# Kernel tuning notes

Measured on AMD Instinct MI355X. Metric: run time of the kernel, lower is better.

The kernel has to match this reference:

```python
import jax, jax.numpy as jnp
import numpy as np

B, N, C, H = 4, 2048, 768, 12
D = C // H  # head_dim = 64

def setup_inputs() -> dict:
    key = jax.random.key(0)
    ks = jax.random.split(key, 6)
    s = 0.02
    return {
        "img_tokens": jax.random.normal(ks[0], (B, N, C), jnp.float32),
        "ln_gamma": jnp.ones((C,), jnp.float32),
        "ln_beta": jnp.zeros((C,), jnp.float32),
        "w_qkv": jax.random.normal(ks[1], (C, 3 * C), jnp.float32) * s,
        "w_out": jax.random.normal(ks[2], (C, C), jnp.float32) * s,
        "b_out": jnp.zeros((C,), jnp.float32),
    }

def reference(img_tokens, ln_gamma, ln_beta, w_qkv, w_out, b_out):
    x = img_tokens
    # LayerNorm over channel dim
    mu = jnp.mean(x, axis=-1, keepdims=True)
    var = jnp.var(x, axis=-1, keepdims=True)
    xn = (x - mu) * jax.lax.rsqrt(var + 1e-5) * ln_gamma + ln_beta
    qkv = xn @ w_qkv                      # [B, N, 3C]
    q, k, v = jnp.split(qkv, 3, axis=-1)
    def heads(t):                          # [B, N, C] -> [B, H, N, D]
        return t.reshape(B, N, H, D).transpose(0, 2, 1, 3)
    q, k, v = heads(q), heads(k), heads(v)
    scale = 1.0 / np.sqrt(D).astype(np.float32)
    scores = jnp.einsum('bhnd,bhmd->bhnm', q, k) * scale  # [B, H, N, N]
    attn = jax.nn.softmax(scores, axis=-1)
    out = jnp.einsum('bhnm,bhmd->bhnd', attn, v)          # [B, H, N, D]
    out = out.transpose(0, 2, 1, 3).reshape(B, N, C)
    out = out @ w_out + b_out
    return out + img_tokens
```

## Files before the change

kernel.cpp:

```cpp
#include <hip/hip_runtime.h>


typedef __bf16 bf16x8 __attribute__((ext_vector_type(8)));
typedef float  f32x4  __attribute__((ext_vector_type(4)));

#define MFMA16(a,b,c) __builtin_amdgcn_mfma_f32_16x16x32_bf16((a),(b),(c),0,0,0)

__device__ inline f32x4 zero4() { f32x4 z = {0.f,0.f,0.f,0.f}; return z; }

__device__ inline void gll16(const __bf16* g, __bf16* l) {
  __builtin_amdgcn_global_load_lds((const __attribute__((address_space(1))) unsigned int*)g,
                                   (__attribute__((address_space(3))) unsigned int*)l,
                                   16, 0, 0);
}

__device__ inline __bf16 bf16_trunc(float f) {
  const unsigned int u = __builtin_bit_cast(unsigned int, f);
  return __builtin_bit_cast(__bf16, (unsigned short)(u >> 16));
}

__global__ __launch_bounds__(256) void ln_kernel(const float* __restrict__ x,
                                                 const float* __restrict__ g,
                                                 const float* __restrict__ bt,
                                                 __bf16* __restrict__ xn) {
  const int row = blockIdx.x;
  const int tid = threadIdx.x;
  const float* xr = x + (size_t)row * 768;
  float v[3]; float s = 0.f, ss = 0.f;
  #pragma unroll
  for (int i = 0; i < 3; ++i) { float f = xr[tid + 256*i]; v[i] = f; s += f; ss += f*f; }
  #pragma unroll
  for (int m = 32; m >= 1; m >>= 1) { s += __shfl_xor(s, m, 64); ss += __shfl_xor(ss, m, 64); }
  __shared__ float red[8];
  const int wave = tid >> 6;
  if ((tid & 63) == 0) { red[wave] = s; red[4 + wave] = ss; }
  __syncthreads();
  s  = red[0] + red[1] + red[2] + red[3];
  ss = red[4] + red[5] + red[6] + red[7];
  const float mu  = s * (1.f/768.f);
  const float var = ss * (1.f/768.f) - mu*mu;
  const float inv = rsqrtf(var + 1e-5f);
  __bf16* xo = xn + (size_t)row * 768;
  #pragma unroll
  for (int i = 0; i < 3; ++i) {
    const int c0 = tid + 256*i;
    xo[c0] = (__bf16)((v[i] - mu) * inv * g[c0] + bt[c0]);
  }
}

__global__ __launch_bounds__(256) void transpose_kernel(const float* __restrict__ in,
                                                        __bf16* __restrict__ out,
                                                        int R, int C) {
  __shared__ float t[32][33];
  const int tx = threadIdx.x & 31, ty = threadIdx.x >> 5;
  const int c0 = blockIdx.x * 32, r0 = blockIdx.y * 32;
  #pragma unroll
  for (int p = 0; p < 4; ++p) t[ty + 8*p][tx] = in[(size_t)(r0 + ty + 8*p) * C + c0 + tx];
  __syncthreads();
  #pragma unroll
  for (int p = 0; p < 4; ++p) out[(size_t)(c0 + ty + 8*p) * R + r0 + tx] = (__bf16)t[tx][ty + 8*p];
}

template<int KDIM>
__device__ inline void gemm_mainloop(const __bf16* __restrict__ A, const __bf16* __restrict__ BT,
                                     int bm, int bn, int wave, int lane,
                                     f32x4 acc[4][4], __bf16* Asm, __bf16* Bsm) {
  const int wm = wave >> 1, wn = wave & 1;
  const int lr = lane & 15, lk = lane >> 4;
  for (int k0 = 0; k0 < KDIM; k0 += 64) {
    #pragma unroll
    for (int s2 = 0; s2 < 4; ++s2) {
      const int st = wave * 4 + s2;
      const int rb = st >> 1, kh = st & 1;
      gll16(A  + (size_t)(bm + rb*16 + lr) * KDIM + k0 + kh*32 + lk*8, Asm + st*512);
      gll16(BT + (size_t)(bn + rb*16 + lr) * KDIM + k0 + kh*32 + lk*8, Bsm + st*512);
    }
    __builtin_amdgcn_s_waitcnt(0);
    __syncthreads();
    #pragma unroll
    for (int ks = 0; ks < 2; ++ks) {
      bf16x8 a[4], b[4];
      #pragma unroll
      for (int mt = 0; mt < 4; ++mt) a[mt] = *(const bf16x8*)(Asm + ((wm*4+mt)*2+ks)*512 + lane*8);
      #pragma unroll
      for (int nt = 0; nt < 4; ++nt) b[nt] = *(const bf16x8*)(Bsm + ((wn*4+nt)*2+ks)*512 + lane*8);
      #pragma unroll
      for (int mt = 0; mt < 4; ++mt)
        #pragma unroll
        for (int nt = 0; nt < 4; ++nt)
          acc[mt][nt] = MFMA16(a[mt], b[nt], acc[mt][nt]);
    }
    __syncthreads();
  }
}

__global__ __launch_bounds__(256) void gemm_qkv_kernel(const __bf16* __restrict__ A,
                                                       const __bf16* __restrict__ BT,
                                                       __bf16* __restrict__ q,
                                                       __bf16* __restrict__ k,
                                                       __bf16* __restrict__ vt) {
  __shared__ __align__(16) __bf16 smem[2*8192];
  __bf16* Asm = smem;
  __bf16* Bsm = smem + 8192;
  const int lane = threadIdx.x & 63, wave = threadIdx.x >> 6;
  const int bm = blockIdx.y * 128, bn = blockIdx.x * 128;
  f32x4 acc[4][4];
  #pragma unroll
  for (int i = 0; i < 4; ++i)
    #pragma unroll
    for (int j = 0; j < 4; ++j) acc[i][j] = zero4();
  gemm_mainloop<768>(A, BT, bm, bn, wave, lane, acc, Asm, Bsm);
  const int wm = wave >> 1, wn = wave & 1;
  const int quad = lane >> 4, c = lane & 15;
  if (bn < 1536) {
    const float qscale = 0.125f * 1.44269504088896f;
    #pragma unroll
    for (int mt = 0; mt < 4; ++mt)
      #pragma unroll
      for (int nt = 0; nt < 4; ++nt) {
        const int col = bn + wn*64 + nt*16 + c;
        const int which = col >= 768 ? 1 : 0;
        const int within = col - which*768;
        const int h = within >> 6, d = within & 63;
        #pragma unroll
        for (int r = 0; r < 4; ++r) {
          const int row = bm + wm*64 + mt*16 + quad*4 + r;
          const int b = row >> 11, n = row & 2047;
          const float vv = acc[mt][nt][r];
          const size_t idx = ((size_t)(b*12 + h) * 2048 + n) * 64 + d;
          if (which == 0) q[idx] = (__bf16)(vv * qscale);
          else            k[idx] = (__bf16)vv;
        }
      }
  } else {
    __syncthreads();
    #pragma unroll
    for (int mt = 0; mt < 4; ++mt)
      #pragma unroll
      for (int nt = 0; nt < 4; ++nt) {
        const int lcol = wn*64 + nt*16 + c;
        #pragma unroll
        for (int r = 0; r < 4; ++r) {
          const int lrow = wm*64 + mt*16 + quad*4 + r;
          smem[lrow*66 + lcol] = (__bf16)acc[mt][nt][r];
        }
      }
    __syncthreads();
    const int b = bm >> 11, n0 = bm & 2047;
    const int vo = bn - 1536;
    const int n = threadIdx.x & 127;
    const int csel = threadIdx.x >> 7;
    #pragma unroll
    for (int pass = 0; pass < 64; ++pass) {
      const int lc = pass*2 + csel;
      const int gcol = vo + lc;
      const int h = gcol >> 6, d = gcol & 63;
      vt[((size_t)(b*12 + h)*64 + d)*2048 + n0 + n] = smem[n*66 + lc];
    }
  }
}

__global__ __launch_bounds__(256) void gemm_out_kernel(const __bf16* __restrict__ A,
                                                       const __bf16* __restrict__ BT,
                                                       const float* __restrict__ bias,
                                                       const float* __restrict__ resid,
                                                       float* __restrict__ out) {
  __shared__ __align__(16) __bf16 Asm[16*512];
  __shared__ __align__(16) __bf16 Bsm[16*512];
  const int lane = threadIdx.x & 63, wave = threadIdx.x >> 6;
  const int bm = blockIdx.y * 128, bn = blockIdx.x * 128;
  f32x4 acc[4][4];
  #pragma unroll
  for (int i = 0; i < 4; ++i)
    #pragma unroll
    for (int j = 0; j < 4; ++j) acc[i][j] = zero4();
  gemm_mainloop<768>(A, BT, bm, bn, wave, lane, acc, Asm, Bsm);
  const int wm = wave >> 1, wn = wave & 1;
  const int quad = lane >> 4, c = lane & 15;
  #pragma unroll
  for (int mt = 0; mt < 4; ++mt)
    #pragma unroll
    for (int nt = 0; nt < 4; ++nt) {
      const int col = bn + wn*64 + nt*16 + c;
      #pragma unroll
      for (int r = 0; r < 4; ++r) {
        const int row = bm + wm*64 + mt*16 + quad*4 + r;
        out[(size_t)row*768 + col] = acc[mt][nt][r] + bias[col] + resid[(size_t)row*768 + col];
      }
    }
}

__global__ __launch_bounds__(256) void attn_kernel(const __bf16* __restrict__ q,
                                                   const __bf16* __restrict__ k,
                                                   const __bf16* __restrict__ vt,
                                                   __bf16* __restrict__ o) {
  const int xcd = blockIdx.x & 7, i = blockIdx.x >> 3;
  const int bh = xcd * 6 + (i >> 4);
  const int qt = i & 15;
  const int lane = threadIdx.x & 63, wave = threadIdx.x >> 6;
  const int c = lane & 15, quad = lane >> 4;
  const int lr = lane & 15, lk = lane >> 4;
  const int q0 = qt*128 + wave*32;

  const __bf16* qb = q  + ((size_t)bh*2048 + q0) * 64;
  const __bf16* kb = k  + (size_t)bh * 2048 * 64;
  const __bf16* vb = vt + (size_t)bh * 64 * 2048;

  __shared__ __align__(16) __bf16 Ksm[2][4096];
  __shared__ __align__(16) __bf16 Vsm[2][4096];
  __shared__ __align__(16) __bf16 plds[4][1024];
  __bf16* myp = plds[wave];

  bf16x8 aq[2][2];
  #pragma unroll
  for (int rg = 0; rg < 2; ++rg) {
    aq[rg][0] = *(const bf16x8*)(qb + (size_t)(rg*16 + c)*64 + quad*8);
    aq[rg][1] = *(const bf16x8*)(qb + (size_t)(rg*16 + c)*64 + 32 + quad*8);
  }

  float cl[2][4];
  f32x4 od[2][4];
  #pragma unroll
  for (int rg = 0; rg < 2; ++rg)
    #pragma unroll
    for (int r = 0; r < 4; ++r) { cl[rg][r] = 0.f; od[rg][r] = zero4(); }

  auto stage = [&](int it) {
    const int kt = it * 64;
    __bf16* Ks = Ksm[it & 1];
    __bf16* Vs = Vsm[it & 1];
    gll16(kb + (size_t)(kt + wave*16 + lr) * 64 + lk*8,        Ks + (wave*2+0)*512);
    gll16(kb + (size_t)(kt + wave*16 + lr) * 64 + 32 + lk*8,   Ks + (wave*2+1)*512);
    gll16(vb + (size_t)(wave*16 + lr) * 2048 + kt + lk*8,      Vs + (wave*2+0)*512);
    gll16(vb + (size_t)(wave*16 + lr) * 2048 + kt + 32 + lk*8, Vs + (wave*2+1)*512);
  };

  stage(0);
  stage(1);

  const int sl = lane ^ ((lane >> 3) & 7);

  for (int it = 0; it < 32; ++it) {
    const __bf16* Ks = Ksm[it & 1];
    const __bf16* Vs = Vsm[it & 1];
    if (it < 31) asm volatile("s_waitcnt vmcnt(4)" ::: "memory");
    else         asm volatile("s_waitcnt vmcnt(0)" ::: "memory");
    asm volatile("s_barrier" ::: "memory");
    #pragma unroll
    for (int ch = 0; ch < 2; ++ch) {
      f32x4 s0[2], s1[2];
      #pragma unroll
      for (int t2 = 0; t2 < 2; ++t2) {
        const int t = ch*2 + t2;
        const bf16x8 b0 = *(const bf16x8*)(Ks + (t*2+0)*512 + lane*8);
        const bf16x8 b1 = *(const bf16x8*)(Ks + (t*2+1)*512 + lane*8);
        f32x4 z0 = zero4(), z1 = zero4();
        z0 = MFMA16(aq[0][0], b0, z0); z0 = MFMA16(aq[0][1], b1, z0);
        z1 = MFMA16(aq[1][0], b0, z1); z1 = MFMA16(aq[1][1], b1, z1);
        s0[t2] = z0; s1[t2] = z1;
      }
      #pragma unroll
      for (int t2 = 0; t2 < 2; ++t2) {
        const int kk = t2*16 + c;
        const int k8 = kk >> 3, j = kk & 7;
        #pragma unroll
        for (int r = 0; r < 4; ++r) {
          const int row = quad*4 + r;
          const int b = k8*16 + row;
          const int sb = b ^ ((b >> 3) & 7);
          const float p0 = __builtin_amdgcn_exp2f(s0[t2][r]);
          const float p1 = __builtin_amdgcn_exp2f(s1[t2][r]);
          cl[0][r] += p0; cl[1][r] += p1;
          myp[sb*8 + j]       = bf16_trunc(p0);
          myp[512 + sb*8 + j] = bf16_trunc(p1);
        }
      }
      asm volatile("s_waitcnt lgkmcnt(0)" ::: "memory");
      const bf16x8 ap0 = *(const bf16x8*)(myp + sl*8);
      const bf16x8 ap1 = *(const bf16x8*)(myp + 512 + sl*8);
      asm volatile("" ::: "memory");
      #pragma unroll
      for (int dt = 0; dt < 4; ++dt) {
        const bf16x8 bv = *(const bf16x8*)(Vs + (dt*2+ch)*512 + lane*8);
        od[0][dt] = MFMA16(ap0, bv, od[0][dt]);
        od[1][dt] = MFMA16(ap1, bv, od[1][dt]);
      }
    }
    asm volatile("s_barrier" ::: "memory");
    if (it + 2 < 32) stage(it + 2);
  }
  const int b = bh / 12, h = bh % 12;
  #pragma unroll
  for (int rg = 0; rg < 2; ++rg) {
    float rl[4];
    #pragma unroll
    for (int r = 0; r < 4; ++r) {
      float v0 = cl[rg][r];
      v0 += __shfl_xor(v0, 1); v0 += __shfl_xor(v0, 2);
      v0 += __shfl_xor(v0, 4); v0 += __shfl_xor(v0, 8);
      rl[r] = 1.f / v0;
    }
    #pragma unroll
    for (int dt = 0; dt < 4; ++dt)
      #pragma unroll
      for (int r = 0; r < 4; ++r) {
        const int n = q0 + rg*16 + quad*4 + r;
        const int col = h*64 + dt*16 + c;
        o[((size_t)b*2048 + n)*768 + col] = (__bf16)(od[rg][dt][r] * rl[r]);
      }
  }
}

extern "C" void kernel_launch(void* const* d_in, const int* in_sizes, int n_in,
                              void* d_out, int out_size, void* d_ws, size_t ws_size,
                              hipStream_t stream) {
  const float* img   = (const float*)d_in[0];
  const float* gamma = (const float*)d_in[1];
  const float* beta  = (const float*)d_in[2];
  const float* wqkv  = (const float*)d_in[3];
  const float* wout  = (const float*)d_in[4];
  const float* bout  = (const float*)d_in[5];
  float* out = (float*)d_out;

  __bf16* ws = (__bf16*)d_ws;
  size_t off = 0;
  __bf16* xn    = ws + off; off += (size_t)8192*768;
  __bf16* wqkvT = ws + off; off += (size_t)2304*768;
  __bf16* woutT = ws + off; off += (size_t)768*768;
  __bf16* qs    = ws + off; off += (size_t)48*2048*64;
  __bf16* ks    = ws + off; off += (size_t)48*2048*64;
  __bf16* vts   = ws + off; off += (size_t)48*64*2048;
  __bf16* os    = ws + off; off += (size_t)8192*768;

  ln_kernel<<<8192, 256, 0, stream>>>(img, gamma, beta, xn);
  transpose_kernel<<<dim3(72, 24), 256, 0, stream>>>(wqkv, wqkvT, 768, 2304);
  transpose_kernel<<<dim3(24, 24), 256, 0, stream>>>(wout, woutT, 768, 768);
  gemm_qkv_kernel<<<dim3(18, 64), 256, 0, stream>>>(xn, wqkvT, qs, ks, vts);
  attn_kernel<<<768, 256, 0, stream>>>(qs, ks, vts, os);
  gemm_out_kernel<<<dim3(6, 64), 256, 0, stream>>>(os, woutT, bout, img, out);
}
```

Before: 272.0 us.

## Keep softmax probabilities in registers via transposed QK MFMA and permlane swaps

Swaps the MFMA operand order for Q·K^T so each lane holds scores for one query row across consecutive keys. The probabilities are then packed to bf16 with v_cvt_pk_bf16_f32 and moved into the A-operand layout of the PV MFMA with permlane32/16 swaps. This drops the per-wave LDS round trip (scattered stores, lgkmcnt wait, reload) and the scratch LDS buffer. The row-sum reduction is also reorganized to a single accumulator per row group with cross-quad shuffles. Rounding changes from truncation to round-to-nearest, and the permlane mapping must match the MFMA operand layout exactly.

```diff
diff --git a/kernel.cpp b/kernel.cpp
--- a/kernel.cpp
+++ b/kernel.cpp
@@ -3,6 +3,7 @@
 
 typedef __bf16 bf16x8 __attribute__((ext_vector_type(8)));
 typedef float  f32x4  __attribute__((ext_vector_type(4)));
+typedef unsigned int u32x4 __attribute__((ext_vector_type(4)));
 
 #define MFMA16(a,b,c) __builtin_amdgcn_mfma_f32_16x16x32_bf16((a),(b),(c),0,0,0)
 
@@ -14,9 +15,16 @@
                                    16, 0, 0);
 }
 
-__device__ inline __bf16 bf16_trunc(float f) {
-  const unsigned int u = __builtin_bit_cast(unsigned int, f);
-  return __builtin_bit_cast(__bf16, (unsigned short)(u >> 16));
+__device__ inline unsigned cvt_pk_bf16(float lo, float hi) {
+  unsigned r;
+  asm("v_cvt_pk_bf16_f32 %0, %1, %2" : "=v"(r) : "v"(lo), "v"(hi));
+  return r;
+}
+__device__ inline void permlane32_swap(unsigned &a, unsigned &b) {
+  asm("v_permlane32_swap_b32 %0, %1" : "+v"(a), "+v"(b));
+}
+__device__ inline void permlane16_swap(unsigned &a, unsigned &b) {
+  asm("v_permlane16_swap_b32 %0, %1" : "+v"(a), "+v"(b));
 }
 
 __global__ __launch_bounds__(256) void ln_kernel(const float* __restrict__ x,
@@ -208,8 +216,6 @@
 
   __shared__ __align__(16) __bf16 Ksm[2][4096];
   __shared__ __align__(16) __bf16 Vsm[2][4096];
-  __shared__ __align__(16) __bf16 plds[4][1024];
-  __bf16* myp = plds[wave];
 
   bf16x8 aq[2][2];
   #pragma unroll
@@ -218,12 +224,14 @@
     aq[rg][1] = *(const bf16x8*)(qb + (size_t)(rg*16 + c)*64 + 32 + quad*8);
   }
 
-  float cl[2][4];
+  float cl[2];
   f32x4 od[2][4];
   #pragma unroll
-  for (int rg = 0; rg < 2; ++rg)
-    #pragma unroll
-    for (int r = 0; r < 4; ++r) { cl[rg][r] = 0.f; od[rg][r] = zero4(); }
+  for (int rg = 0; rg < 2; ++rg) {
+    cl[rg] = 0.f;
+    #pragma unroll
+    for (int r = 0; r < 4; ++r) od[rg][r] = zero4();
+  }
 
   auto stage = [&](int it) {
     const int kt = it * 64;
@@ -238,8 +246,6 @@
   stage(0);
   stage(1);
 
-  const int sl = lane ^ ((lane >> 3) & 7);
-
   for (int it = 0; it < 32; ++it) {
     const __bf16* Ks = Ksm[it & 1];
     const __bf16* Vs = Vsm[it & 1];
@@ -248,42 +254,43 @@
     asm volatile("s_barrier" ::: "memory");
     #pragma unroll
     for (int ch = 0; ch < 2; ++ch) {
-      f32x4 s0[2], s1[2];
+      unsigned pk[2][2][2];
       #pragma unroll
       for (int t2 = 0; t2 < 2; ++t2) {
         const int t = ch*2 + t2;
-        const bf16x8 b0 = *(const bf16x8*)(Ks + (t*2+0)*512 + lane*8);
-        const bf16x8 b1 = *(const bf16x8*)(Ks + (t*2+1)*512 + lane*8);
-        f32x4 z0 = zero4(), z1 = zero4();
-        z0 = MFMA16(aq[0][0], b0, z0); z0 = MFMA16(aq[0][1], b1, z0);
-        z1 = MFMA16(aq[1][0], b0, z1); z1 = MFMA16(aq[1][1], b1, z1);
-        s0[t2] = z0; s1[t2] = z1;
-      }
-      #pragma unroll
-      for (int t2 = 0; t2 < 2; ++t2) {
-        const int kk = t2*16 + c;
-        const int k8 = kk >> 3, j = kk & 7;
+        const bf16x8 ka0 = *(const bf16x8*)(Ks + (t*2+0)*512 + lane*8);
+        const bf16x8 ka1 = *(const bf16x8*)(Ks + (t*2+1)*512 + lane*8);
         #pragma unroll
-        for (int r = 0; r < 4; ++r) {
-          const int row = quad*4 + r;
-          const int b = k8*16 + row;
-          const int sb = b ^ ((b >> 3) & 7);
-          const float p0 = __builtin_amdgcn_exp2f(s0[t2][r]);
-          const float p1 = __builtin_amdgcn_exp2f(s1[t2][r]);
-          cl[0][r] += p0; cl[1][r] += p1;
-          myp[sb*8 + j]       = bf16_trunc(p0);
-          myp[512 + sb*8 + j] = bf16_trunc(p1);
+        for (int rg = 0; rg < 2; ++rg) {
+          f32x4 z = zero4();
+          z = MFMA16(ka0, aq[rg][0], z);
+          z = MFMA16(ka1, aq[rg][1], z);
+          const float p0 = __builtin_amdgcn_exp2f(z[0]);
+          const float p1 = __builtin_amdgcn_exp2f(z[1]);
+          const float p2 = __builtin_amdgcn_exp2f(z[2]);
+          const float p3 = __builtin_amdgcn_exp2f(z[3]);
+          cl[rg] += (p0 + p1) + (p2 + p3);
+          pk[rg][t2][0] = cvt_pk_bf16(p0, p1);
+          pk[rg][t2][1] = cvt_pk_bf16(p2, p3);
         }
       }
-      asm volatile("s_waitcnt lgkmcnt(0)" ::: "memory");
-      const bf16x8 ap0 = *(const bf16x8*)(myp + sl*8);
-      const bf16x8 ap1 = *(const bf16x8*)(myp + 512 + sl*8);
-      asm volatile("" ::: "memory");
+      bf16x8 pa[2];
+      #pragma unroll
+      for (int rg = 0; rg < 2; ++rg) {
+        unsigned s0 = pk[rg][0][0], s2 = pk[rg][1][0];
+        permlane32_swap(s0, s2);
+        permlane16_swap(s0, s2);
+        unsigned s1 = pk[rg][0][1], s3 = pk[rg][1][1];
+        permlane32_swap(s1, s3);
+        permlane16_swap(s1, s3);
+        u32x4 w4; w4.x = s0; w4.y = s1; w4.z = s2; w4.w = s3;
+        pa[rg] = __builtin_bit_cast(bf16x8, w4);
+      }
       #pragma unroll
       for (int dt = 0; dt < 4; ++dt) {
         const bf16x8 bv = *(const bf16x8*)(Vs + (dt*2+ch)*512 + lane*8);
-        od[0][dt] = MFMA16(ap0, bv, od[0][dt]);
-        od[1][dt] = MFMA16(ap1, bv, od[1][dt]);
+        od[0][dt] = MFMA16(pa[0], bv, od[0][dt]);
+        od[1][dt] = MFMA16(pa[1], bv, od[1][dt]);
       }
     }
     asm volatile("s_barrier" ::: "memory");
@@ -292,14 +299,12 @@
   const int b = bh / 12, h = bh % 12;
   #pragma unroll
   for (int rg = 0; rg < 2; ++rg) {
+    float s = cl[rg];
+    s += __shfl_xor(s, 16, 64);
+    s += __shfl_xor(s, 32, 64);
     float rl[4];
     #pragma unroll
-    for (int r = 0; r < 4; ++r) {
-      float v0 = cl[rg][r];
-      v0 += __shfl_xor(v0, 1); v0 += __shfl_xor(v0, 2);
-      v0 += __shfl_xor(v0, 4); v0 += __shfl_xor(v0, 8);
-      rl[r] = 1.f / v0;
-    }
+    for (int r = 0; r < 4; ++r) rl[r] = 1.f / __shfl(s, quad*4 + r, 64);
     #pragma unroll
     for (int dt = 0; dt < 4; ++dt)
       #pragma unroll
```

New measurement: 272.3 us. Within noise of the previous version (+0.1%).
